# Kernel tuning notes

Measured on AMD Instinct MI355X. Metric: run time of the kernel, lower is better.

The kernel has to match this reference:

```python
import jax, jax.numpy as jnp
import numpy as np

N_EMBD = 768
N_HEAD = 8
HEAD_DIM = N_EMBD // N_HEAD


def setup_inputs() -> dict:
    key = jax.random.key(0)
    k1, k2, k3, k4, k5 = jax.random.split(key, 5)
    B, T, C = 8, 1024, N_EMBD
    scale = 0.02
    return {
        "x": jax.random.normal(k1, (B, T, C), dtype=jnp.float32),
        "W_attn": jax.random.normal(k2, (C, 3 * C), dtype=jnp.float32) * scale,
        "b_attn": jnp.zeros((3 * C,), dtype=jnp.float32),
        "W_proj": jax.random.normal(k3, (C, C), dtype=jnp.float32) * scale,
        "b_proj": jnp.zeros((C,), dtype=jnp.float32),
    }


def reference(x, W_attn, b_attn, W_proj, b_proj):
    B, T, C = x.shape
    H, D = N_HEAD, HEAD_DIM
    qkv = x @ W_attn + b_attn                      # [B,T,3C]
    q, k, v = jnp.split(qkv, 3, axis=-1)
    # [B,H,T,D]
    q = q.reshape(B, T, H, D).transpose(0, 2, 1, 3)
    k = k.reshape(B, T, H, D).transpose(0, 2, 1, 3)
    v = v.reshape(B, T, H, D).transpose(0, 2, 1, 3)
    att = jnp.einsum("bhqd,bhkd->bhqk", q, k) * (1.0 / jnp.sqrt(jnp.float32(D)))
    causal = jnp.tril(jnp.ones((T, T), dtype=bool))
    att = jnp.where(causal[None, None], att, jnp.float32(-jnp.inf))
    att = jax.nn.softmax(att, axis=-1)
    y = jnp.einsum("bhqk,bhkd->bhqd", att, v)      # [B,H,T,D]
    y = y.transpose(0, 2, 1, 3).reshape(B, T, C)
    return y @ W_proj + b_proj
```

## Files before the change

kernel.cpp:

```cpp
#include <hip/hip_runtime.h>
#include <math.h>

#define B_ 8
#define T_ 1024
#define C_ 768
#define H_ 8
#define D_ 96
#define M_ (B_ * T_)
#define N1_ (3 * C_)
#define KD_ 768

typedef __bf16 bf16x8 __attribute__((ext_vector_type(8)));
typedef float f32x4 __attribute__((ext_vector_type(4)));
typedef float f32x16 __attribute__((ext_vector_type(16)));

__device__ __forceinline__ unsigned short f2bf(float f) {
  unsigned int u = __float_as_uint(f);
  u += 0x7FFF + ((u >> 16) & 1);
  return (unsigned short)(u >> 16);
}

__device__ __forceinline__ void load_lds16(const void* g, void* l) {
  __builtin_amdgcn_global_load_lds(
      (const __attribute__((address_space(1))) unsigned int*)g,
      (__attribute__((address_space(3))) unsigned int*)l, 16, 0, 0);
}

__global__ __launch_bounds__(256) void cvt_bf16_kernel(
    const float* __restrict__ in, unsigned short* __restrict__ out, int n) {
  int i = (blockIdx.x * 256 + threadIdx.x) * 4;
  if (i + 3 < n) {
    float4 v = *(const float4*)(in + i);
    ushort4 o;
    o.x = f2bf(v.x); o.y = f2bf(v.y); o.z = f2bf(v.z); o.w = f2bf(v.w);
    *(ushort4*)(out + i) = o;
  }
}

__global__ __launch_bounds__(256) void w_transpose2_kernel(
    const float* __restrict__ Wa, unsigned short* __restrict__ WaT,
    const float* __restrict__ Wp, unsigned short* __restrict__ WpT) {
  __shared__ float Lt[32][33];
  int bid = blockIdx.x;
  const float* W; unsigned short* WT; int Nd;
  if (bid < 1728) { W = Wa; WT = WaT; Nd = N1_; }
  else            { W = Wp; WT = WpT; Nd = C_; bid -= 1728; }
  const int r0 = (bid % 24) * 32;
  const int c0 = (bid / 24) * 32;
#pragma unroll
  for (int i = 0; i < 4; ++i) {
    int e = threadIdx.x + 256 * i;
    int r = e >> 5, c = e & 31;
    Lt[r][c] = W[(size_t)(r0 + r) * Nd + c0 + c];
  }
  __syncthreads();
#pragma unroll
  for (int i = 0; i < 4; ++i) {
    int e = threadIdx.x + 256 * i;
    int rr = e >> 5, cc = e & 31;
    WT[(size_t)(c0 + rr) * KD_ + r0 + cc] = f2bf(Lt[cc][rr]);
  }
}

template <int WM32, bool OUTF32, bool VSCAT>
__global__ __launch_bounds__(256) void gemm_mfma_kernel(
    const unsigned short* __restrict__ A, const unsigned short* __restrict__ Bt,
    const float* __restrict__ bias, void* __restrict__ Cout,
    unsigned short* __restrict__ vt, int N,
    int sc_lim, float sc, int mmask, int mshift) {
  constexpr int AS2 = 2 * WM32;
  constexpr int NC  = (AS2 + 4) * 2;
  constexpr int CPW = NC / 4;
  __shared__ __align__(16) unsigned short Sb[2][NC * 512];
  const int tid = threadIdx.x;
  const int w = tid >> 6, l = tid & 63;
  const int l31 = l & 31, lh = l >> 5;
  const int bid = blockIdx.x;
  const int m0 = (bid & mmask) * (AS2 * 32), n0 = (bid >> mshift) * 128;
  const int wrb = (w >> 1) * WM32;
  const int wnb = (w & 1) * 2;

  f32x16 acc[WM32][2];
#pragma unroll
  for (int i = 0; i < WM32; ++i)
#pragma unroll
    for (int j = 0; j < 2; ++j)
#pragma unroll
      for (int r = 0; r < 16; ++r) acc[i][j][r] = 0.f;

  const unsigned short* gp[CPW];
#pragma unroll
  for (int i = 0; i < CPW; ++i) {
    const int c = w * CPW + i;
    const int pr = c >> 1, kh = c & 1;
    gp[i] = (pr < AS2)
        ? A  + (size_t)(m0 + pr * 32 + l31) * KD_ + kh * 16 + lh * 8
        : Bt + (size_t)(n0 + (pr - AS2) * 32 + l31) * KD_ + kh * 16 + lh * 8;
  }

#pragma unroll
  for (int i = 0; i < CPW; ++i) {
    load_lds16(gp[i], &Sb[0][(w * CPW + i) * 512]);
    gp[i] += 32;
  }

  int cur = 0;
  for (int k0 = 0; k0 < KD_; k0 += 32) {
    __syncthreads();
    if (k0 + 32 < KD_) {
#pragma unroll
      for (int i = 0; i < CPW; ++i) {
        load_lds16(gp[i], &Sb[cur ^ 1][(w * CPW + i) * 512]);
        gp[i] += 32;
      }
    }
#pragma unroll
    for (int kh = 0; kh < 2; ++kh) {
      bf16x8 af[WM32], bfr[2];
#pragma unroll
      for (int mi = 0; mi < WM32; ++mi)
        af[mi] = *(const bf16x8*)&Sb[cur][((wrb + mi) * 2 + kh) * 512 + l * 8];
#pragma unroll
      for (int ni = 0; ni < 2; ++ni)
        bfr[ni] = *(const bf16x8*)&Sb[cur][((AS2 + wnb + ni) * 2 + kh) * 512 + l * 8];
#pragma unroll
      for (int mi = 0; mi < WM32; ++mi)
#pragma unroll
        for (int ni = 0; ni < 2; ++ni)
          acc[mi][ni] = __builtin_amdgcn_mfma_f32_32x32x16_bf16(
              af[mi], bfr[ni], acc[mi][ni], 0, 0, 0);
    }
    cur ^= 1;
  }

  const bool vblock = VSCAT && (n0 >= 1536);
#pragma unroll
  for (int mi = 0; mi < WM32; ++mi) {
    const int rowb = m0 + (wrb + mi) * 32 + 4 * lh;
#pragma unroll
    for (int ni = 0; ni < 2; ++ni) {
      const int col = n0 + (wnb + ni) * 32 + l31;
      const float bv = bias[col];
      if (!vblock) {
        const float mul = (col < sc_lim) ? sc : 1.f;
#pragma unroll
        for (int r = 0; r < 16; ++r) {
          const int row = rowb + (r & 3) + 8 * (r >> 2);
          float v = (acc[mi][ni][r] + bv) * mul;
          if (OUTF32)
            ((float*)Cout)[(size_t)row * N + col] = v;
          else
            ((unsigned short*)Cout)[(size_t)row * N + col] = f2bf(v);
        }
      } else {
        const int x = col - 1536;
        const int h = x / 96, d = x % 96;
#pragma unroll
        for (int r = 0; r < 16; ++r) {
          const int row = rowb + (r & 3) + 8 * (r >> 2);
          const int bb = row >> 10, t = row & 1023;
          vt[((size_t)(bb * H_ + h) * D_ + d) * T_ + t] = f2bf(acc[mi][ni][r] + bv);
        }
      }
    }
  }
}

__global__ __launch_bounds__(256) void attn_mfma_kernel(
    const unsigned short* __restrict__ qkv,
    const unsigned short* __restrict__ vt,
    unsigned short* __restrict__ y) {
  __shared__ __align__(16) unsigned short KV[2][24 * 512];
  __shared__ __align__(16) unsigned short Pt[4][16][72];

  const int tid = threadIdx.x;
  const int w = tid >> 6, l = tid & 63;
  const int lm = l & 15, lq = l >> 4;
  const int bh = blockIdx.x & 63, pi = blockIdx.x >> 6;
  const int b = bh >> 3, h = bh & 7;
  const size_t bT = (size_t)b * T_;

  bf16x8 onef;
#pragma unroll
  for (int i = 0; i < 8; ++i) onef[i] = (__bf16)1.0f;

  auto issue = [&](int j0, int buf) {
#pragma unroll
    for (int i = 0; i < 6; ++i) {
      const int c = w * 6 + i;
      const unsigned short* g;
      if (c < 12) {
        const int kc = c >> 2, nb = c & 3;
        g = qkv + (bT + j0 + nb * 16 + lm) * N1_ + C_ + h * D_ + kc * 32 + lq * 8;
      } else {
        const int cv = c - 12;
        const int db = cv >> 1, vc = cv & 1;
        g = vt + ((size_t)bh * D_ + db * 16 + lm) * T_ + j0 + vc * 32 + lq * 8;
      }
      load_lds16(g, &KV[buf][c * 512]);
    }
  };

  int cur = 0;
  issue(0, 0);

  for (int half = 0; half < 2; ++half) {
    const int qt = half ? (15 - pi) : pi;
    const int q0 = qt * 64;

    bf16x8 qf[3];
    {
      const unsigned short* qp =
          qkv + (bT + q0 + w * 16 + lm) * N1_ + h * D_ + lq * 8;
      qf[0] = *(const bf16x8*)(qp);
      qf[1] = *(const bf16x8*)(qp + 32);
      qf[2] = *(const bf16x8*)(qp + 64);
    }
    f32x4 o[7];
#pragma unroll
    for (int i = 0; i < 7; ++i) o[i] = (f32x4){0.f, 0.f, 0.f, 0.f};

    for (int jt = 0; jt <= qt; ++jt) {
      __syncthreads();
      if (jt < qt)          issue((jt + 1) * 64, cur ^ 1);
      else if (half == 0)   issue(0, cur ^ 1);

      const bool diag = (jt == qt);
#pragma unroll
      for (int nb = 0; nb < 4; ++nb) {
        if (diag && nb > w) {
#pragma unroll
          for (int r = 0; r < 4; ++r)
            Pt[w][lq * 4 + r][nb * 16 + lm] = 0;
          continue;
        }
        f32x4 a = (f32x4){0.f, 0.f, 0.f, 0.f};
#pragma unroll
        for (int kc = 0; kc < 3; ++kc) {
          bf16x8 kf = *(const bf16x8*)&KV[cur][(kc * 4 + nb) * 512 + l * 8];
          a = __builtin_amdgcn_mfma_f32_16x16x32_bf16(qf[kc], kf, a, 0, 0, 0);
        }
#pragma unroll
        for (int r = 0; r < 4; ++r) {
          float s = a[r];
          if (diag && (nb * 16 + lm > w * 16 + lq * 4 + r)) s = -INFINITY;
          Pt[w][lq * 4 + r][nb * 16 + lm] = f2bf(__expf(s));
        }
      }

      bf16x8 pf0 = *(const bf16x8*)&Pt[w][lm][lq * 8];
      bf16x8 pf1 = *(const bf16x8*)&Pt[w][lm][32 + lq * 8];
#pragma unroll
      for (int db = 0; db < 6; ++db) {
        bf16x8 vf0 = *(const bf16x8*)&KV[cur][(12 + db * 2 + 0) * 512 + l * 8];
        bf16x8 vf1 = *(const bf16x8*)&KV[cur][(12 + db * 2 + 1) * 512 + l * 8];
        o[db] = __builtin_amdgcn_mfma_f32_16x16x32_bf16(pf0, vf0, o[db], 0, 0, 0);
        o[db] = __builtin_amdgcn_mfma_f32_16x16x32_bf16(pf1, vf1, o[db], 0, 0, 0);
      }
      o[6] = __builtin_amdgcn_mfma_f32_16x16x32_bf16(pf0, onef, o[6], 0, 0, 0);
      o[6] = __builtin_amdgcn_mfma_f32_16x16x32_bf16(pf1, onef, o[6], 0, 0, 0);
      cur ^= 1;
    }

#pragma unroll
    for (int r = 0; r < 4; ++r) {
      const float inv = 1.f / o[6][r];
      const size_t row = bT + q0 + w * 16 + lq * 4 + r;
#pragma unroll
      for (int db = 0; db < 6; ++db)
        y[row * C_ + h * D_ + db * 16 + lm] = f2bf(o[db][r] * inv);
    }
  }
}

extern "C" void kernel_launch(void* const* d_in, const int* in_sizes, int n_in,
                              void* d_out, int out_size, void* d_ws, size_t ws_size,
                              hipStream_t stream) {
  const float* x      = (const float*)d_in[0];
  const float* W_attn = (const float*)d_in[1];
  const float* b_attn = (const float*)d_in[2];
  const float* W_proj = (const float*)d_in[3];
  const float* b_proj = (const float*)d_in[4];
  float* out = (float*)d_out;

  char* ws = (char*)d_ws;
  unsigned short* xb  = (unsigned short*)(ws);
  unsigned short* WaT = (unsigned short*)(ws + 12582912);
  unsigned short* WpT = (unsigned short*)(ws + 16121856);
  unsigned short* qkv = (unsigned short*)(ws + 17301504);
  unsigned short* vt  = (unsigned short*)(ws + 55050240);
  unsigned short* yb  = (unsigned short*)(ws + 67633152);

  const float qscale = 0.10206207261596577f;

  cvt_bf16_kernel<<<(M_ * C_) / 1024, 256, 0, stream>>>(x, xb, M_ * C_);
  w_transpose2_kernel<<<2304, 256, 0, stream>>>(W_attn, WaT, W_proj, WpT);

  gemm_mfma_kernel<2, false, true><<<(N1_ / 128) * (M_ / 128), 256, 0, stream>>>(
      xb, WaT, b_attn, qkv, vt, N1_, C_, qscale, 63, 6);
  attn_mfma_kernel<<<8 * B_ * H_, 256, 0, stream>>>(qkv, vt, yb);
  gemm_mfma_kernel<1, true, false><<<(C_ / 128) * (M_ / 64), 256, 0, stream>>>(
      yb, WpT, b_proj, out, nullptr, C_, 0, 1.f, 127, 7);
}
```

Baseline: 221.2 us.

## Warp-specialize GEMM into producer and consumer waves with LDS flag sync

Replaces the double-buffered GEMM with a warp-specialized version. Two producer waves load tiles from global memory into registers and store them into a 3-stage LDS ring. Four MFMA consumer waves spin on LDS flag counters instead of block-wide barriers. The goal is to overlap global loads with MFMA compute and drop __syncthreads. In exchange it adds spin-wait polling, register-staged loads in place of direct global-to-LDS loads, more LDS per block, and possible memory-ordering hazards because the flags use volatile LDS with no fences.

After: 397.1 us. 1.8x slower.

```diff
diff --git a/kernel.cpp b/kernel.cpp
--- a/kernel.cpp
+++ b/kernel.cpp
@@ -63,104 +63,137 @@
 }
 
 template <int WM32, bool OUTF32, bool VSCAT>
-__global__ __launch_bounds__(256) void gemm_mfma_kernel(
+__global__ __launch_bounds__(384) void gemm_pc_kernel(
     const unsigned short* __restrict__ A, const unsigned short* __restrict__ Bt,
     const float* __restrict__ bias, void* __restrict__ Cout,
     unsigned short* __restrict__ vt, int N,
     int sc_lim, float sc, int mmask, int mshift) {
-  constexpr int AS2 = 2 * WM32;
-  constexpr int NC  = (AS2 + 4) * 2;
-  constexpr int CPW = NC / 4;
-  __shared__ __align__(16) unsigned short Sb[2][NC * 512];
+  constexpr int AS2  = 2 * WM32;
+  constexpr int NCH  = AS2 * 2 + 8;
+  constexpr int S    = 3;
+  constexpr int CPP  = NCH / 2;
+  constexpr int NITER = KD_ / 32;
+  __shared__ __align__(16) unsigned short Sb[S][NCH * 512];
+  __shared__ int flg[2 * S];
+  __shared__ int done[4];
+
   const int tid = threadIdx.x;
   const int w = tid >> 6, l = tid & 63;
   const int l31 = l & 31, lh = l >> 5;
   const int bid = blockIdx.x;
   const int m0 = (bid & mmask) * (AS2 * 32), n0 = (bid >> mshift) * 128;
-  const int wrb = (w >> 1) * WM32;
-  const int wnb = (w & 1) * 2;
-
-  f32x16 acc[WM32][2];
-#pragma unroll
-  for (int i = 0; i < WM32; ++i)
-#pragma unroll
-    for (int j = 0; j < 2; ++j)
-#pragma unroll
-      for (int r = 0; r < 16; ++r) acc[i][j][r] = 0.f;
-
-  const unsigned short* gp[CPW];
-#pragma unroll
-  for (int i = 0; i < CPW; ++i) {
-    const int c = w * CPW + i;
-    const int pr = c >> 1, kh = c & 1;
-    gp[i] = (pr < AS2)
-        ? A  + (size_t)(m0 + pr * 32 + l31) * KD_ + kh * 16 + lh * 8
-        : Bt + (size_t)(n0 + (pr - AS2) * 32 + l31) * KD_ + kh * 16 + lh * 8;
-  }
-
-#pragma unroll
-  for (int i = 0; i < CPW; ++i) {
-    load_lds16(gp[i], &Sb[0][(w * CPW + i) * 512]);
-    gp[i] += 32;
-  }
-
-  int cur = 0;
-  for (int k0 = 0; k0 < KD_; k0 += 32) {
-    __syncthreads();
-    if (k0 + 32 < KD_) {
-#pragma unroll
-      for (int i = 0; i < CPW; ++i) {
-        load_lds16(gp[i], &Sb[cur ^ 1][(w * CPW + i) * 512]);
-        gp[i] += 32;
-      }
-    }
-#pragma unroll
-    for (int kh = 0; kh < 2; ++kh) {
-      bf16x8 af[WM32], bfr[2];
-#pragma unroll
-      for (int mi = 0; mi < WM32; ++mi)
-        af[mi] = *(const bf16x8*)&Sb[cur][((wrb + mi) * 2 + kh) * 512 + l * 8];
-#pragma unroll
-      for (int ni = 0; ni < 2; ++ni)
-        bfr[ni] = *(const bf16x8*)&Sb[cur][((AS2 + wnb + ni) * 2 + kh) * 512 + l * 8];
-#pragma unroll
-      for (int mi = 0; mi < WM32; ++mi)
+
+  if (tid < 2 * S) flg[tid] = 0;
+  if (tid < 4) done[tid] = 0;
+  __syncthreads();
+
+  if (w < 4) {
+    const int wrb = (w >> 1) * WM32;
+    const int wnb = (w & 1) * 2;
+    f32x16 acc[WM32][2];
+#pragma unroll
+    for (int i = 0; i < WM32; ++i)
+#pragma unroll
+      for (int j = 0; j < 2; ++j)
+#pragma unroll
+        for (int r = 0; r < 16; ++r) acc[i][j][r] = 0.f;
+
+    for (int k = 0; k < NITER; ++k) {
+      const int s = k % S;
+      while (*(volatile int*)&flg[0 * S + s] < k + 1) __builtin_amdgcn_s_sleep(1);
+      while (*(volatile int*)&flg[1 * S + s] < k + 1) __builtin_amdgcn_s_sleep(1);
+      __asm__ __volatile__("" ::: "memory");
+#pragma unroll
+      for (int kh = 0; kh < 2; ++kh) {
+        bf16x8 af[WM32], bfr[2];
+#pragma unroll
+        for (int mi = 0; mi < WM32; ++mi)
+          af[mi] = *(const bf16x8*)&Sb[s][((wrb + mi) * 2 + kh) * 512 + l * 8];
 #pragma unroll
         for (int ni = 0; ni < 2; ++ni)
-          acc[mi][ni] = __builtin_amdgcn_mfma_f32_32x32x16_bf16(
-              af[mi], bfr[ni], acc[mi][ni], 0, 0, 0);
-    }
-    cur ^= 1;
-  }
-
-  const bool vblock = VSCAT && (n0 >= 1536);
-#pragma unroll
-  for (int mi = 0; mi < WM32; ++mi) {
-    const int rowb = m0 + (wrb + mi) * 32 + 4 * lh;
-#pragma unroll
-    for (int ni = 0; ni < 2; ++ni) {
-      const int col = n0 + (wnb + ni) * 32 + l31;
-      const float bv = bias[col];
-      if (!vblock) {
-        const float mul = (col < sc_lim) ? sc : 1.f;
-#pragma unroll
-        for (int r = 0; r < 16; ++r) {
-          const int row = rowb + (r & 3) + 8 * (r >> 2);
-          float v = (acc[mi][ni][r] + bv) * mul;
-          if (OUTF32)
-            ((float*)Cout)[(size_t)row * N + col] = v;
-          else
-            ((unsigned short*)Cout)[(size_t)row * N + col] = f2bf(v);
-        }
-      } else {
-        const int x = col - 1536;
-        const int h = x / 96, d = x % 96;
-#pragma unroll
-        for (int r = 0; r < 16; ++r) {
-          const int row = rowb + (r & 3) + 8 * (r >> 2);
-          const int bb = row >> 10, t = row & 1023;
-          vt[((size_t)(bb * H_ + h) * D_ + d) * T_ + t] = f2bf(acc[mi][ni][r] + bv);
-        }
+          bfr[ni] = *(const bf16x8*)&Sb[s][((AS2 + wnb + ni) * 2 + kh) * 512 + l * 8];
+#pragma unroll
+        for (int mi = 0; mi < WM32; ++mi)
+#pragma unroll
+          for (int ni = 0; ni < 2; ++ni)
+            acc[mi][ni] = __builtin_amdgcn_mfma_f32_32x32x16_bf16(
+                af[mi], bfr[ni], acc[mi][ni], 0, 0, 0);
+      }
+      __asm__ __volatile__("" ::: "memory");
+      if (l == 0) *(volatile int*)&done[w] = k + 1;
+    }
+
+    const bool vblock = VSCAT && (n0 >= 1536);
+#pragma unroll
+    for (int mi = 0; mi < WM32; ++mi) {
+      const int rowb = m0 + (wrb + mi) * 32 + 4 * lh;
+#pragma unroll
+      for (int ni = 0; ni < 2; ++ni) {
+        const int col = n0 + (wnb + ni) * 32 + l31;
+        const float bv = bias[col];
+        if (!vblock) {
+          const float mul = (col < sc_lim) ? sc : 1.f;
+#pragma unroll
+          for (int r = 0; r < 16; ++r) {
+            const int row = rowb + (r & 3) + 8 * (r >> 2);
+            float v = (acc[mi][ni][r] + bv) * mul;
+            if (OUTF32)
+              ((float*)Cout)[(size_t)row * N + col] = v;
+            else
+              ((unsigned short*)Cout)[(size_t)row * N + col] = f2bf(v);
+          }
+        } else {
+          const int x = col - 1536;
+          const int h = x / 96, d = x % 96;
+#pragma unroll
+          for (int r = 0; r < 16; ++r) {
+            const int row = rowb + (r & 3) + 8 * (r >> 2);
+            const int bb = row >> 10, t = row & 1023;
+            vt[((size_t)(bb * H_ + h) * D_ + d) * T_ + t] =
+                f2bf(acc[mi][ni][r] + bv);
+          }
+        }
+      }
+    }
+  } else {
+    const int pw = w - 4;
+    const unsigned short* gp[CPP];
+#pragma unroll
+    for (int i = 0; i < CPP; ++i) {
+      const int c = pw * CPP + i;
+      const int pr = c >> 1, kh = c & 1;
+      gp[i] = (pr < AS2)
+          ? A  + (size_t)(m0 + pr * 32 + l31) * KD_ + kh * 16 + lh * 8
+          : Bt + (size_t)(n0 + (pr - AS2) * 32 + l31) * KD_ + kh * 16 + lh * 8;
+    }
+    uint4 rv[2][CPP];
+#pragma unroll
+    for (int i = 0; i < CPP; ++i) { rv[0][i] = *(const uint4*)gp[i]; gp[i] += 32; }
+#pragma unroll
+    for (int i = 0; i < CPP; ++i) { rv[1][i] = *(const uint4*)gp[i]; gp[i] += 32; }
+
+    for (int k = 0; k < NITER; ++k) {
+      const int s = k % S;
+      if (k >= S) {
+        const int need = k - S + 1;
+        for (;;) {
+          int d0 = *(volatile int*)&done[0];
+          int d1 = *(volatile int*)&done[1];
+          int d2 = *(volatile int*)&done[2];
+          int d3 = *(volatile int*)&done[3];
+          if (min(min(d0, d1), min(d2, d3)) >= need) break;
+          __builtin_amdgcn_s_sleep(1);
+        }
+      }
+      __asm__ __volatile__("" ::: "memory");
+#pragma unroll
+      for (int i = 0; i < CPP; ++i)
+        *(uint4*)&Sb[s][(pw * CPP + i) * 512 + l * 8] = rv[k & 1][i];
+      __asm__ __volatile__("" ::: "memory");
+      if (l == 0) *(volatile int*)&flg[pw * S + s] = k + 1;
+      if (k + 2 < NITER) {
+#pragma unroll
+        for (int i = 0; i < CPP; ++i) { rv[k & 1][i] = *(const uint4*)gp[i]; gp[i] += 32; }
       }
     }
   }
@@ -296,9 +329,9 @@
   cvt_bf16_kernel<<<(M_ * C_) / 1024, 256, 0, stream>>>(x, xb, M_ * C_);
   w_transpose2_kernel<<<2304, 256, 0, stream>>>(W_attn, WaT, W_proj, WpT);
 
-  gemm_mfma_kernel<2, false, true><<<(N1_ / 128) * (M_ / 128), 256, 0, stream>>>(
+  gemm_pc_kernel<2, false, true><<<(N1_ / 128) * (M_ / 128), 384, 0, stream>>>(
       xb, WaT, b_attn, qkv, vt, N1_, C_, qscale, 63, 6);
   attn_mfma_kernel<<<8 * B_ * H_, 256, 0, stream>>>(qkv, vt, yb);
-  gemm_mfma_kernel<1, true, false><<<(C_ / 128) * (M_ / 64), 256, 0, stream>>>(
+  gemm_pc_kernel<1, true, false><<<(C_ / 128) * (M_ / 64), 384, 0, stream>>>(
       yb, WpT, b_proj, out, nullptr, C_, 0, 1.f, 127, 7);
 }
```

## Stage GEMM tiles through registers with two-deep prefetch and fully unrolled K loop

Applied to the files above, without the earlier changes.

The GEMM main loop no longer uses direct global-to-LDS loads. It now loads tiles into registers two K-steps ahead, writes them into a double-buffered LDS tile, and synchronises with a single custom lgkmcnt-wait-plus-barrier per step. The 24-step K loop is fully unrolled, and the launch bounds ask for two workgroups per CU. This aims to hide global latency better and shorten the barrier path, at the cost of more VGPRs, larger code and extra LDS write instructions.

Result: slower. 363.6 us (+64.4%).

```diff
diff --git a/kernel.cpp b/kernel.cpp
--- a/kernel.cpp
+++ b/kernel.cpp
@@ -9,6 +9,7 @@
 #define M_ (B_ * T_)
 #define N1_ (3 * C_)
 #define KD_ 768
+#define NIT 24
 
 typedef __bf16 bf16x8 __attribute__((ext_vector_type(8)));
 typedef float f32x4 __attribute__((ext_vector_type(4)));
@@ -24,6 +25,10 @@
   __builtin_amdgcn_global_load_lds(
       (const __attribute__((address_space(1))) unsigned int*)g,
       (__attribute__((address_space(3))) unsigned int*)l, 16, 0, 0);
+}
+
+__device__ __forceinline__ void wg_barrier_lds() {
+  __asm__ __volatile__("s_waitcnt lgkmcnt(0)\n\ts_barrier" ::: "memory");
 }
 
 __global__ __launch_bounds__(256) void cvt_bf16_kernel(
@@ -63,15 +68,15 @@
 }
 
 template <int WM32, bool OUTF32, bool VSCAT>
-__global__ __launch_bounds__(256) void gemm_mfma_kernel(
+__global__ __launch_bounds__(256, 2) void gemm_mfma_kernel(
     const unsigned short* __restrict__ A, const unsigned short* __restrict__ Bt,
     const float* __restrict__ bias, void* __restrict__ Cout,
     unsigned short* __restrict__ vt, int N,
     int sc_lim, float sc, int mmask, int mshift) {
   constexpr int AS2 = 2 * WM32;
-  constexpr int NC  = (AS2 + 4) * 2;
-  constexpr int CPW = NC / 4;
-  __shared__ __align__(16) unsigned short Sb[2][NC * 512];
+  constexpr int NCH = AS2 * 2 + 8;
+  constexpr int CPW = NCH / 4;
+  __shared__ __align__(16) unsigned short Sb[2][NCH * 512];
   const int tid = threadIdx.x;
   const int w = tid >> 6, l = tid & 63;
   const int l31 = l & 31, lh = l >> 5;
@@ -98,31 +103,33 @@
         : Bt + (size_t)(n0 + (pr - AS2) * 32 + l31) * KD_ + kh * 16 + lh * 8;
   }
 
-#pragma unroll
-  for (int i = 0; i < CPW; ++i) {
-    load_lds16(gp[i], &Sb[0][(w * CPW + i) * 512]);
-    gp[i] += 32;
-  }
-
-  int cur = 0;
-  for (int k0 = 0; k0 < KD_; k0 += 32) {
-    __syncthreads();
-    if (k0 + 32 < KD_) {
-#pragma unroll
-      for (int i = 0; i < CPW; ++i) {
-        load_lds16(gp[i], &Sb[cur ^ 1][(w * CPW + i) * 512]);
-        gp[i] += 32;
-      }
-    }
+  uint4 rg[3][CPW];
+#pragma unroll
+  for (int i = 0; i < CPW; ++i) { rg[0][i] = *(const uint4*)gp[i]; gp[i] += 32; }
+#pragma unroll
+  for (int i = 0; i < CPW; ++i) { rg[1][i] = *(const uint4*)gp[i]; gp[i] += 32; }
+
+#pragma unroll
+  for (int k = 0; k < NIT; ++k) {
+    unsigned short* sb = Sb[k & 1];
+    const int cs = k % 3, ns = (k + 2) % 3;
+#pragma unroll
+    for (int i = 0; i < CPW; ++i)
+      *(uint4*)&sb[(w * CPW + i) * 512 + l * 8] = rg[cs][i];
+    if (k + 2 < NIT) {
+#pragma unroll
+      for (int i = 0; i < CPW; ++i) { rg[ns][i] = *(const uint4*)gp[i]; gp[i] += 32; }
+    }
+    wg_barrier_lds();
 #pragma unroll
     for (int kh = 0; kh < 2; ++kh) {
       bf16x8 af[WM32], bfr[2];
 #pragma unroll
       for (int mi = 0; mi < WM32; ++mi)
-        af[mi] = *(const bf16x8*)&Sb[cur][((wrb + mi) * 2 + kh) * 512 + l * 8];
+        af[mi] = *(const bf16x8*)&sb[((wrb + mi) * 2 + kh) * 512 + l * 8];
 #pragma unroll
       for (int ni = 0; ni < 2; ++ni)
-        bfr[ni] = *(const bf16x8*)&Sb[cur][((AS2 + wnb + ni) * 2 + kh) * 512 + l * 8];
+        bfr[ni] = *(const bf16x8*)&sb[((AS2 + wnb + ni) * 2 + kh) * 512 + l * 8];
 #pragma unroll
       for (int mi = 0; mi < WM32; ++mi)
 #pragma unroll
@@ -130,7 +137,6 @@
           acc[mi][ni] = __builtin_amdgcn_mfma_f32_32x32x16_bf16(
               af[mi], bfr[ni], acc[mi][ni], 0, 0, 0);
     }
-    cur ^= 1;
   }
 
   const bool vblock = VSCAT && (n0 >= 1536);
@@ -159,7 +165,8 @@
         for (int r = 0; r < 16; ++r) {
           const int row = rowb + (r & 3) + 8 * (r >> 2);
           const int bb = row >> 10, t = row & 1023;
-          vt[((size_t)(bb * H_ + h) * D_ + d) * T_ + t] = f2bf(acc[mi][ni][r] + bv);
+          vt[((size_t)(bb * H_ + h) * D_ + d) * T_ + t] =
+              f2bf(acc[mi][ni][r] + bv);
         }
       }
     }
```

## Shrink GEMM tiles to smaller blocks with 2-wave and 1-wave kernels

Applied to the files above, without the earlier changes.

The QKV GEMM moves from 128x128 tiles on 256 threads to 64x128 tiles on 128 threads. The output projection uses a new single-wave kernel with 64x64 tiles. That kernel double-buffers and uses an explicit vmcnt wait instead of __syncthreads. The aim is more blocks for better CU occupancy and load balance, plus lower barrier overhead. The cost is less data reuse per block and more global/L2 traffic.

Result: slower. 248.7 us (+12.4%).

```diff
diff --git a/kernel.cpp b/kernel.cpp
--- a/kernel.cpp
+++ b/kernel.cpp
@@ -9,6 +9,7 @@
 #define M_ (B_ * T_)
 #define N1_ (3 * C_)
 #define KD_ 768
+#define NIT 24
 
 typedef __bf16 bf16x8 __attribute__((ext_vector_type(8)));
 typedef float f32x4 __attribute__((ext_vector_type(4)));
@@ -62,27 +63,24 @@
   }
 }
 
-template <int WM32, bool OUTF32, bool VSCAT>
-__global__ __launch_bounds__(256) void gemm_mfma_kernel(
+template <bool OUTF32, bool VSCAT>
+__global__ __launch_bounds__(128) void gemm2w_kernel(
     const unsigned short* __restrict__ A, const unsigned short* __restrict__ Bt,
     const float* __restrict__ bias, void* __restrict__ Cout,
     unsigned short* __restrict__ vt, int N,
     int sc_lim, float sc, int mmask, int mshift) {
-  constexpr int AS2 = 2 * WM32;
-  constexpr int NC  = (AS2 + 4) * 2;
-  constexpr int CPW = NC / 4;
-  __shared__ __align__(16) unsigned short Sb[2][NC * 512];
+  constexpr int NCH = 12;
+  constexpr int CPW = 6;
+  __shared__ __align__(16) unsigned short Sb[2][NCH * 512];
   const int tid = threadIdx.x;
   const int w = tid >> 6, l = tid & 63;
   const int l31 = l & 31, lh = l >> 5;
   const int bid = blockIdx.x;
-  const int m0 = (bid & mmask) * (AS2 * 32), n0 = (bid >> mshift) * 128;
-  const int wrb = (w >> 1) * WM32;
-  const int wnb = (w & 1) * 2;
-
-  f32x16 acc[WM32][2];
-#pragma unroll
-  for (int i = 0; i < WM32; ++i)
+  const int m0 = (bid & mmask) * 64, n0 = (bid >> mshift) * 128;
+
+  f32x16 acc[2][2];
+#pragma unroll
+  for (int i = 0; i < 2; ++i)
 #pragma unroll
     for (int j = 0; j < 2; ++j)
 #pragma unroll
@@ -93,9 +91,9 @@
   for (int i = 0; i < CPW; ++i) {
     const int c = w * CPW + i;
     const int pr = c >> 1, kh = c & 1;
-    gp[i] = (pr < AS2)
+    gp[i] = (pr < 2)
         ? A  + (size_t)(m0 + pr * 32 + l31) * KD_ + kh * 16 + lh * 8
-        : Bt + (size_t)(n0 + (pr - AS2) * 32 + l31) * KD_ + kh * 16 + lh * 8;
+        : Bt + (size_t)(n0 + (pr - 2) * 32 + l31) * KD_ + kh * 16 + lh * 8;
   }
 
 #pragma unroll
@@ -116,15 +114,15 @@
     }
 #pragma unroll
     for (int kh = 0; kh < 2; ++kh) {
-      bf16x8 af[WM32], bfr[2];
-#pragma unroll
-      for (int mi = 0; mi < WM32; ++mi)
-        af[mi] = *(const bf16x8*)&Sb[cur][((wrb + mi) * 2 + kh) * 512 + l * 8];
+      bf16x8 af[2], bfr[2];
+#pragma unroll
+      for (int mi = 0; mi < 2; ++mi)
+        af[mi] = *(const bf16x8*)&Sb[cur][(mi * 2 + kh) * 512 + l * 8];
 #pragma unroll
       for (int ni = 0; ni < 2; ++ni)
-        bfr[ni] = *(const bf16x8*)&Sb[cur][((AS2 + wnb + ni) * 2 + kh) * 512 + l * 8];
-#pragma unroll
-      for (int mi = 0; mi < WM32; ++mi)
+        bfr[ni] = *(const bf16x8*)&Sb[cur][(4 + (w * 2 + ni) * 2 + kh) * 512 + l * 8];
+#pragma unroll
+      for (int mi = 0; mi < 2; ++mi)
 #pragma unroll
         for (int ni = 0; ni < 2; ++ni)
           acc[mi][ni] = __builtin_amdgcn_mfma_f32_32x32x16_bf16(
@@ -135,11 +133,11 @@
 
   const bool vblock = VSCAT && (n0 >= 1536);
 #pragma unroll
-  for (int mi = 0; mi < WM32; ++mi) {
-    const int rowb = m0 + (wrb + mi) * 32 + 4 * lh;
+  for (int mi = 0; mi < 2; ++mi) {
+    const int rowb = m0 + mi * 32 + 4 * lh;
 #pragma unroll
     for (int ni = 0; ni < 2; ++ni) {
-      const int col = n0 + (wnb + ni) * 32 + l31;
+      const int col = n0 + (w * 2 + ni) * 32 + l31;
       const float bv = bias[col];
       if (!vblock) {
         const float mul = (col < sc_lim) ? sc : 1.f;
@@ -159,8 +157,90 @@
         for (int r = 0; r < 16; ++r) {
           const int row = rowb + (r & 3) + 8 * (r >> 2);
           const int bb = row >> 10, t = row & 1023;
-          vt[((size_t)(bb * H_ + h) * D_ + d) * T_ + t] = f2bf(acc[mi][ni][r] + bv);
-        }
+          vt[((size_t)(bb * H_ + h) * D_ + d) * T_ + t] =
+              f2bf(acc[mi][ni][r] + bv);
+        }
+      }
+    }
+  }
+}
+
+__global__ __launch_bounds__(64) void gemm1w_kernel(
+    const unsigned short* __restrict__ A, const unsigned short* __restrict__ Bt,
+    const float* __restrict__ bias, float* __restrict__ Cout, int N,
+    int mmask, int mshift) {
+  constexpr int NCH = 8;
+  __shared__ __align__(16) unsigned short Sb[2][NCH * 512];
+  const int l = threadIdx.x;
+  const int l31 = l & 31, lh = l >> 5;
+  const int bid = blockIdx.x;
+  const int m0 = (bid & mmask) * 64, n0 = (bid >> mshift) * 64;
+
+  f32x16 acc[2][2];
+#pragma unroll
+  for (int i = 0; i < 2; ++i)
+#pragma unroll
+    for (int j = 0; j < 2; ++j)
+#pragma unroll
+      for (int r = 0; r < 16; ++r) acc[i][j][r] = 0.f;
+
+  const unsigned short* gp[NCH];
+#pragma unroll
+  for (int c = 0; c < NCH; ++c) {
+    const int pr = c >> 1, kh = c & 1;
+    gp[c] = (pr < 2)
+        ? A  + (size_t)(m0 + pr * 32 + l31) * KD_ + kh * 16 + lh * 8
+        : Bt + (size_t)(n0 + (pr - 2) * 32 + l31) * KD_ + kh * 16 + lh * 8;
+  }
+
+#pragma unroll
+  for (int c = 0; c < NCH; ++c) {
+    load_lds16(gp[c], &Sb[0][c * 512]);
+    gp[c] += 32;
+  }
+
+  for (int k = 0; k < NIT; ++k) {
+    const unsigned short* sb = Sb[k & 1];
+    if (k + 1 < NIT) {
+      unsigned short* nb = Sb[(k + 1) & 1];
+#pragma unroll
+      for (int c = 0; c < NCH; ++c) {
+        load_lds16(gp[c], &nb[c * 512]);
+        gp[c] += 32;
+      }
+      __asm__ __volatile__("s_waitcnt vmcnt(8)" ::: "memory");
+    } else {
+      __asm__ __volatile__("s_waitcnt vmcnt(0)" ::: "memory");
+    }
+#pragma unroll
+    for (int kh = 0; kh < 2; ++kh) {
+      bf16x8 af[2], bfr[2];
+#pragma unroll
+      for (int mi = 0; mi < 2; ++mi)
+        af[mi] = *(const bf16x8*)&sb[(mi * 2 + kh) * 512 + l * 8];
+#pragma unroll
+      for (int ni = 0; ni < 2; ++ni)
+        bfr[ni] = *(const bf16x8*)&sb[(4 + ni * 2 + kh) * 512 + l * 8];
+#pragma unroll
+      for (int mi = 0; mi < 2; ++mi)
+#pragma unroll
+        for (int ni = 0; ni < 2; ++ni)
+          acc[mi][ni] = __builtin_amdgcn_mfma_f32_32x32x16_bf16(
+              af[mi], bfr[ni], acc[mi][ni], 0, 0, 0);
+    }
+  }
+
+#pragma unroll
+  for (int mi = 0; mi < 2; ++mi) {
+    const int rowb = m0 + mi * 32 + 4 * lh;
+#pragma unroll
+    for (int ni = 0; ni < 2; ++ni) {
+      const int col = n0 + ni * 32 + l31;
+      const float bv = bias[col];
+#pragma unroll
+      for (int r = 0; r < 16; ++r) {
+        const int row = rowb + (r & 3) + 8 * (r >> 2);
+        Cout[(size_t)row * N + col] = acc[mi][ni][r] + bv;
       }
     }
   }
@@ -296,9 +376,9 @@
   cvt_bf16_kernel<<<(M_ * C_) / 1024, 256, 0, stream>>>(x, xb, M_ * C_);
   w_transpose2_kernel<<<2304, 256, 0, stream>>>(W_attn, WaT, W_proj, WpT);
 
-  gemm_mfma_kernel<2, false, true><<<(N1_ / 128) * (M_ / 128), 256, 0, stream>>>(
-      xb, WaT, b_attn, qkv, vt, N1_, C_, qscale, 63, 6);
+  gemm2w_kernel<false, true><<<(N1_ / 128) * (M_ / 64), 128, 0, stream>>>(
+      xb, WaT, b_attn, qkv, vt, N1_, C_, qscale, 127, 7);
   attn_mfma_kernel<<<8 * B_ * H_, 256, 0, stream>>>(qkv, vt, yb);
-  gemm_mfma_kernel<1, true, false><<<(C_ / 128) * (M_ / 64), 256, 0, stream>>>(
-      yb, WpT, b_proj, out, nullptr, C_, 0, 1.f, 127, 7);
-}
+  gemm1w_kernel<<<(C_ / 64) * (M_ / 64), 64, 0, stream>>>(
+      yb, WpT, b_proj, out, C_, 127, 7);
+}
```
